# Kernel optimization log

Measured on AMD Instinct MI355X. Metric: run time of the kernel, lower is better.

The kernel has to match this reference:

```python
import jax, jax.numpy as jnp
import numpy as np
from jax import lax

HIDDEN = 30
NUM_CLASSES = 10
SEQ = 784
BATCH = 16384


def setup_inputs() -> dict:
    key = jax.random.key(0)
    k = jax.random.split(key, 6)
    s_ih = 1.0  # fan_in = 1
    s_hh = 1.0 / np.sqrt(HIDDEN)
    s_lin = 1.0 / np.sqrt(HIDDEN)
    return {
        "inputs": jax.random.normal(k[0], (BATCH, SEQ), dtype=jnp.float32),
        "W_ih": jax.random.normal(k[1], (HIDDEN, 1), dtype=jnp.float32) * s_ih,
        "W_hh": jax.random.normal(k[2], (HIDDEN, HIDDEN), dtype=jnp.float32) * s_hh,
        "b_mod": jax.random.normal(k[3], (HIDDEN,), dtype=jnp.float32) * 0.1,
        "W_lin": jax.random.normal(k[4], (NUM_CLASSES, HIDDEN), dtype=jnp.float32) * s_lin,
        "b_lin": jax.random.normal(k[5], (NUM_CLASSES,), dtype=jnp.float32) * s_lin,
    }


def reference(inputs, W_ih, W_hh, b_mod, W_lin, b_lin):
    # inputs: [B, 784] pixel-by-pixel sequence. Scan over the 784 time steps.
    B = inputs.shape[0]
    # Precompute the input projection for all steps at once: [784, B, H]
    # (W_ih has shape [H, 1], so x_t @ W_ih.T == x_t[:, None] * W_ih[:, 0])
    x_proj = inputs.T[:, :, None] * W_ih[:, 0][None, None, :]  # [784, B, H]

    def step(h, xp):
        z = xp + h @ W_hh.T  # [B, H]
        # modReLU: sign(z) * relu(|z| + b)
        h_new = jnp.sign(z) * jax.nn.relu(jnp.abs(z) + b_mod)
        return h_new, None

    h0 = jnp.zeros((B, HIDDEN), dtype=inputs.dtype)
    h_final, _ = lax.scan(step, h0, x_proj)
    return h_final @ W_lin.T + b_lin  # [B, 10] logits
```

## Files before the change

### kernel.cpp

```cpp
#include <hip/hip_runtime.h>
#include <stdint.h>

#define HID 30
#define NCLS 10
#define SEQ 784
#define NBATCH 16384
#define TCH 112
#define NSTAGE 7
#define XPAD 116

typedef _Float16 f16x8 __attribute__((ext_vector_type(8)));
typedef _Float16 f16x2 __attribute__((ext_vector_type(2)));
typedef float f32x4 __attribute__((ext_vector_type(4)));
typedef uint32_t u32x4 __attribute__((ext_vector_type(4)));

static __device__ __forceinline__ f16x8 mkfrag16(uint32_t a, uint32_t b, uint32_t c, uint32_t d) {
    u32x4 t = {a, b, c, d};
    return __builtin_bit_cast(f16x8, t);
}

static __device__ __forceinline__ uint32_t pkf16(_Float16 lo, _Float16 hi) {
    f16x2 v = {lo, hi};
    return __builtin_bit_cast(uint32_t, v);
}

static __device__ __forceinline__ uint32_t pk_rne(float a, float b) {
    return pkf16((_Float16)a, (_Float16)b);
}

static __device__ __forceinline__ uint32_t pkrtz(float a, float b) {
    return __builtin_bit_cast(uint32_t, __builtin_amdgcn_cvt_pkrtz(a, b));
}

static __device__ __forceinline__ uint32_t modrelu_pk(uint32_t z, uint32_t bp) {
    const f16x2 zero2 = {(_Float16)0.f, (_Float16)0.f};
    f16x2 t = __builtin_bit_cast(f16x2, z & 0x7FFF7FFFu) + __builtin_bit_cast(f16x2, bp);
    t = __builtin_elementwise_max(t, zero2);
    const uint32_t tb = __builtin_bit_cast(uint32_t, t);
    return (tb & 0x7FFF7FFFu) | (z & 0x80008000u);
}

static __device__ __forceinline__ uint32_t pkmax(uint32_t a, uint32_t b) {
    return __builtin_bit_cast(uint32_t,
        __builtin_elementwise_max(__builtin_bit_cast(f16x2, a), __builtin_bit_cast(f16x2, b)));
}

static __device__ __forceinline__ uint32_t scale_mul(uint32_t v, uint32_t sc32) {
    return __builtin_bit_cast(uint32_t,
        __builtin_bit_cast(f16x2, v) * __builtin_bit_cast(f16x2, sc32));
}

__launch_bounds__(64, 1)
__global__ void rnn_scan_kernel(const float* __restrict__ inp,
                                const float* __restrict__ W_ih,
                                const float* __restrict__ W_hh,
                                const float* __restrict__ b_mod,
                                const float* __restrict__ W_lin,
                                const float* __restrict__ b_lin,
                                float* __restrict__ out)
{
    __shared__ __align__(16) float xs_lds[16 * XPAD];

    const int lane = threadIdx.x;
    const int q = lane >> 4;
    const int n = lane & 15;
    const int b0 = blockIdx.x * 16;

    const int i1 = 8 * (n >> 2) + (n & 3);
    const int i2 = i1 + 4;

    uint32_t a1h[4], a1m[4], a2h[4], a2m[4];
    #pragma unroll
    for (int p = 0; p < 4; ++p) {
        _Float16 h1[2], m1[2], h2[2], m2[2];
        #pragma unroll
        for (int e = 0; e < 2; ++e) {
            const int j = 8 * q + 2 * p + e;
            float w1 = 0.f, w2 = 0.f;
            if (j < HID) {
                w1 = W_hh[i1 * HID + j];
                if (i2 < HID) w2 = W_hh[i2 * HID + j];
            } else if (j == HID) {
                w1 = W_ih[i1];
                if (i2 < HID) w2 = W_ih[i2];
            }
            h1[e] = (_Float16)w1; m1[e] = (_Float16)(w1 - (float)h1[e]);
            h2[e] = (_Float16)w2; m2[e] = (_Float16)(w2 - (float)h2[e]);
        }
        a1h[p] = pkf16(h1[0], h1[1]); a1m[p] = pkf16(m1[0], m1[1]);
        a2h[p] = pkf16(h2[0], h2[1]); a2m[p] = pkf16(m2[0], m2[1]);
    }
    const f16x8 A1h = mkfrag16(a1h[0], a1h[1], a1h[2], a1h[3]);
    const f16x8 A1m = mkfrag16(a1m[0], a1m[1], a1m[2], a1m[3]);
    const f16x8 A2h = mkfrag16(a2h[0], a2h[1], a2h[2], a2h[3]);
    const f16x8 A2m = mkfrag16(a2m[0], a2m[1], a2m[2], a2m[3]);

    uint32_t bSp[4];
    #pragma unroll
    for (int p = 0; p < 4; ++p) {
        const int ja = 8 * q + 2 * p;
        const int jb = ja + 1;
        const float ba = (ja < HID) ? b_mod[ja] : 0.f;
        const float bb = (jb < HID) ? b_mod[jb] : 0.f;
        bSp[p] = pk_rne(ba, bb);
    }

    uint32_t hp[4] = {0u, 0u, 0u, 0u};
    int xinv_e = 0;
    int pend_field = 15;

    const bool isq3 = (q == 3);
    const f32x4 z4 = {0.f, 0.f, 0.f, 0.f};

    auto do8 = [&](const uint32_t* xpk) {
        #pragma unroll
        for (int tt = 0; tt < 8; ++tt) {
            const f16x8 Bh = mkfrag16(hp[0], hp[1], hp[2], hp[3]);
            const f32x4 d1a = __builtin_amdgcn_mfma_f32_16x16x32_f16(A1h, Bh, z4, 0, 0, 0);
            const f32x4 d2a = __builtin_amdgcn_mfma_f32_16x16x32_f16(A2h, Bh, z4, 0, 0, 0);
            const f32x4 d1b = __builtin_amdgcn_mfma_f32_16x16x32_f16(A1m, Bh, z4, 0, 0, 0);
            const f32x4 d2b = __builtin_amdgcn_mfma_f32_16x16x32_f16(A2m, Bh, z4, 0, 0, 0);
            const f32x4 d1 = d1a + d1b;
            const f32x4 d2 = d2a + d2b;
            hp[0] = modrelu_pk(pk_rne(d1[0], d1[1]), bSp[0]);
            hp[1] = modrelu_pk(pk_rne(d1[2], d1[3]), bSp[1]);
            hp[2] = modrelu_pk(pk_rne(d2[0], d2[1]), bSp[2]);
            const uint32_t mr3 = modrelu_pk(pk_rne(d2[2], d2[3]), bSp[3]);
            hp[3] = isq3 ? xpk[(tt + 1) & 7] : mr3;
        }
    };

    for (int s = 0; s < NSTAGE; ++s) {
        #pragma unroll
        for (int r = 0; r < 7; ++r) {
            const int idx = r * 64 + lane;
            const int bl = idx / 28;
            const int t4 = idx % 28;
            const float4 v = *(const float4*)(inp + (size_t)(b0 + bl) * SEQ + s * TCH + t4 * 4);
            *(float4*)(&xs_lds[bl * XPAD + t4 * 4]) = v;
        }
        __syncthreads();

        const float* xrow = &xs_lds[n * XPAD];
        float4 xv0 = *(const float4*)(xrow);
        float4 xv1 = *(const float4*)(xrow + 4);

        for (int t16 = 0; t16 < 7; ++t16) {
            const uint32_t sc32 = (uint32_t)pend_field * 0x04000400u;
            #pragma unroll
            for (int p = 0; p < 4; ++p) hp[p] = scale_mul(hp[p], sc32);
            #pragma unroll
            for (int p = 0; p < 4; ++p) bSp[p] = scale_mul(bSp[p], sc32);
            xinv_e += pend_field - 15;

            const float fac = __uint_as_float((uint32_t)(127 + xinv_e) << 23);

            uint32_t mx;

            {
                const int toff = t16 * 16 + 8;
                const float4 xn0 = *(const float4*)(xrow + toff);
                const float4 xn1 = *(const float4*)(xrow + toff + 4);

                uint32_t xpk[8];
                xpk[0] = pkrtz(xv0.x * fac, 0.f); xpk[1] = pkrtz(xv0.y * fac, 0.f);
                xpk[2] = pkrtz(xv0.z * fac, 0.f); xpk[3] = pkrtz(xv0.w * fac, 0.f);
                xpk[4] = pkrtz(xv1.x * fac, 0.f); xpk[5] = pkrtz(xv1.y * fac, 0.f);
                xpk[6] = pkrtz(xv1.z * fac, 0.f); xpk[7] = pkrtz(xv1.w * fac, 0.f);
                hp[3] = isq3 ? xpk[0] : hp[3];

                mx = pkmax(pkmax(hp[0] & 0x7FFF7FFFu, hp[1] & 0x7FFF7FFFu),
                           pkmax(hp[2] & 0x7FFF7FFFu, hp[3] & 0x7FFF7FFFu));
                const uint32_t sh1 = (uint32_t)__shfl_xor((int)mx, 16);

                do8(xpk);

                mx = pkmax(mx, sh1);
                xv0 = xn0;
                xv1 = xn1;
            }
            const uint32_t sh2 = (uint32_t)__shfl_xor((int)mx, 32);

            {
                const int toff = (t16 < 6) ? (t16 + 1) * 16 : 0;
                const float4 xn0 = *(const float4*)(xrow + toff);
                const float4 xn1 = *(const float4*)(xrow + toff + 4);

                uint32_t xpk[8];
                xpk[0] = pkrtz(xv0.x * fac, 0.f); xpk[1] = pkrtz(xv0.y * fac, 0.f);
                xpk[2] = pkrtz(xv0.z * fac, 0.f); xpk[3] = pkrtz(xv0.w * fac, 0.f);
                xpk[4] = pkrtz(xv1.x * fac, 0.f); xpk[5] = pkrtz(xv1.y * fac, 0.f);
                xpk[6] = pkrtz(xv1.z * fac, 0.f); xpk[7] = pkrtz(xv1.w * fac, 0.f);
                hp[3] = isq3 ? xpk[0] : hp[3];

                do8(xpk);

                xv0 = xn0;
                xv1 = xn1;
            }

            mx = pkmax(mx, sh2);
            const uint32_t e16 = max(mx & 0xFFFFu, mx >> 16);
            const int e_raw = (int)(e16 >> 10);
            pend_field = min(max(25 - e_raw, 1), 20);
        }
        __syncthreads();
    }

    const float S = __uint_as_float((uint32_t)(127 - xinv_e) << 23);
    float hf[8];
    #pragma unroll
    for (int p = 0; p < 4; ++p) {
        const f16x2 v = __builtin_bit_cast(f16x2, hp[p]);
        hf[2 * p] = (float)v.x;
        hf[2 * p + 1] = (float)v.y;
    }
    float acc[NCLS];
    #pragma unroll
    for (int c = 0; c < NCLS; ++c) {
        float p = 0.f;
        #pragma unroll
        for (int k = 0; k < 8; ++k) {
            const int j = 8 * q + k;
            if (j < HID) p += W_lin[c * HID + j] * hf[k];
        }
        p += __shfl_xor(p, 16, 64);
        p += __shfl_xor(p, 32, 64);
        acc[c] = p * S + b_lin[c];
    }
    if (q == 0) {
        #pragma unroll
        for (int c = 0; c < NCLS; ++c)
            out[(size_t)(b0 + n) * NCLS + c] = acc[c];
    }
}

extern "C" void kernel_launch(void* const* d_in, const int* in_sizes, int n_in,
                              void* d_out, int out_size, void* d_ws, size_t ws_size,
                              hipStream_t stream) {
    const float* inp   = (const float*)d_in[0];
    const float* W_ih  = (const float*)d_in[1];
    const float* W_hh  = (const float*)d_in[2];
    const float* b_mod = (const float*)d_in[3];
    const float* W_lin = (const float*)d_in[4];
    const float* b_lin = (const float*)d_in[5];
    float* out = (float*)d_out;

    dim3 grid(NBATCH / 16);
    dim3 block(64);
    hipLaunchKernelGGL(rnn_scan_kernel, grid, block, 0, stream,
                       inp, W_ih, W_hh, b_mod, W_lin, b_lin, out);
}
```

Measured before the change: 191.2 us.

## Split recurrence rows across two waves with per-step LDS hidden-state exchange

Each block now runs two wavefronts. Each wave computes half of the hidden rows, so it issues two chained MFMAs per step instead of four. The new hidden-state halves are swapped through a double-buffered LDS array with a block barrier after every time step. The aim is to shorten the per-step MFMA critical path and double the number of resident waves. The cost is 784 block-wide barriers plus LDS write/read round trips on the serial dependency chain, and the end-of-stage barrier is removed.

```diff
diff --git a/kernel.cpp b/kernel.cpp
--- a/kernel.cpp
+++ b/kernel.cpp
@@ -50,7 +50,7 @@
         __builtin_bit_cast(f16x2, v) * __builtin_bit_cast(f16x2, sc32));
 }
 
-__launch_bounds__(64, 1)
+__launch_bounds__(128, 1)
 __global__ void rnn_scan_kernel(const float* __restrict__ inp,
                                 const float* __restrict__ W_ih,
                                 const float* __restrict__ W_hh,
@@ -60,84 +60,88 @@
                                 float* __restrict__ out)
 {
     __shared__ __align__(16) float xs_lds[16 * XPAD];
-
-    const int lane = threadIdx.x;
+    __shared__ uint32_t ex[2][4][64];
+
+    const int tid  = threadIdx.x;
+    const int wid  = tid >> 6;
+    const int lane = tid & 63;
     const int q = lane >> 4;
     const int n = lane & 15;
     const int b0 = blockIdx.x * 16;
 
-    const int i1 = 8 * (n >> 2) + (n & 3);
-    const int i2 = i1 + 4;
-
-    uint32_t a1h[4], a1m[4], a2h[4], a2m[4];
+    const int irow = 8 * (n >> 2) + (n & 3) + 4 * wid;
+
+    uint32_t ah[4], am[4];
     #pragma unroll
     for (int p = 0; p < 4; ++p) {
-        _Float16 h1[2], m1[2], h2[2], m2[2];
+        _Float16 hh[2], mm[2];
         #pragma unroll
         for (int e = 0; e < 2; ++e) {
             const int j = 8 * q + 2 * p + e;
-            float w1 = 0.f, w2 = 0.f;
-            if (j < HID) {
-                w1 = W_hh[i1 * HID + j];
-                if (i2 < HID) w2 = W_hh[i2 * HID + j];
-            } else if (j == HID) {
-                w1 = W_ih[i1];
-                if (i2 < HID) w2 = W_ih[i2];
-            }
-            h1[e] = (_Float16)w1; m1[e] = (_Float16)(w1 - (float)h1[e]);
-            h2[e] = (_Float16)w2; m2[e] = (_Float16)(w2 - (float)h2[e]);
-        }
-        a1h[p] = pkf16(h1[0], h1[1]); a1m[p] = pkf16(m1[0], m1[1]);
-        a2h[p] = pkf16(h2[0], h2[1]); a2m[p] = pkf16(m2[0], m2[1]);
-    }
-    const f16x8 A1h = mkfrag16(a1h[0], a1h[1], a1h[2], a1h[3]);
-    const f16x8 A1m = mkfrag16(a1m[0], a1m[1], a1m[2], a1m[3]);
-    const f16x8 A2h = mkfrag16(a2h[0], a2h[1], a2h[2], a2h[3]);
-    const f16x8 A2m = mkfrag16(a2m[0], a2m[1], a2m[2], a2m[3]);
-
-    uint32_t bSp[4];
-    #pragma unroll
-    for (int p = 0; p < 4; ++p) {
-        const int ja = 8 * q + 2 * p;
-        const int jb = ja + 1;
-        const float ba = (ja < HID) ? b_mod[ja] : 0.f;
-        const float bb = (jb < HID) ? b_mod[jb] : 0.f;
-        bSp[p] = pk_rne(ba, bb);
-    }
-
-    uint32_t hp[4] = {0u, 0u, 0u, 0u};
+            float w = 0.f;
+            if (irow < HID) {
+                if (j < HID) w = W_hh[irow * HID + j];
+                else if (j == HID) w = W_ih[irow];
+            }
+            hh[e] = (_Float16)w; mm[e] = (_Float16)(w - (float)hh[e]);
+        }
+        ah[p] = pkf16(hh[0], hh[1]); am[p] = pkf16(mm[0], mm[1]);
+    }
+    const f16x8 Ah = mkfrag16(ah[0], ah[1], ah[2], ah[3]);
+    const f16x8 Am = mkfrag16(am[0], am[1], am[2], am[3]);
+
+    uint32_t bS0, bS1;
+    {
+        const int r0 = 8 * q + 4 * wid;
+        const float ba = (r0     < HID) ? b_mod[r0]     : 0.f;
+        const float bb = (r0 + 1 < HID) ? b_mod[r0 + 1] : 0.f;
+        const float bc = (r0 + 2 < HID) ? b_mod[r0 + 2] : 0.f;
+        const float bd = (r0 + 3 < HID) ? b_mod[r0 + 3] : 0.f;
+        bS0 = pk_rne(ba, bb);
+        bS1 = pk_rne(bc, bd);
+    }
+
+    uint32_t B0 = 0u, B1 = 0u, B2 = 0u, B3 = 0u;
+    int par = 0;
     int xinv_e = 0;
     int pend_field = 15;
 
-    const bool isq3 = (q == 3);
+    const bool isq3  = (q == 3);
+    const bool isInj = (wid == 1) && isq3;
     const f32x4 z4 = {0.f, 0.f, 0.f, 0.f};
 
+    auto step = [&](uint32_t xnext) {
+        const f16x8 Bf = mkfrag16(B0, B1, B2, B3);
+        f32x4 d = __builtin_amdgcn_mfma_f32_16x16x32_f16(Ah, Bf, z4, 0, 0, 0);
+        d = __builtin_amdgcn_mfma_f32_16x16x32_f16(Am, Bf, d, 0, 0, 0);
+        const uint32_t u0  = modrelu_pk(pk_rne(d[0], d[1]), bS0);
+        const uint32_t u1m = modrelu_pk(pk_rne(d[2], d[3]), bS1);
+        const uint32_t u1  = isInj ? xnext : u1m;
+        ex[par][2 * wid][lane]     = u0;
+        ex[par][2 * wid + 1][lane] = u1;
+        __syncthreads();
+        B0 = ex[par][0][lane];
+        B1 = ex[par][1][lane];
+        B2 = ex[par][2][lane];
+        B3 = ex[par][3][lane];
+        par ^= 1;
+    };
+
     auto do8 = [&](const uint32_t* xpk) {
         #pragma unroll
-        for (int tt = 0; tt < 8; ++tt) {
-            const f16x8 Bh = mkfrag16(hp[0], hp[1], hp[2], hp[3]);
-            const f32x4 d1a = __builtin_amdgcn_mfma_f32_16x16x32_f16(A1h, Bh, z4, 0, 0, 0);
-            const f32x4 d2a = __builtin_amdgcn_mfma_f32_16x16x32_f16(A2h, Bh, z4, 0, 0, 0);
-            const f32x4 d1b = __builtin_amdgcn_mfma_f32_16x16x32_f16(A1m, Bh, z4, 0, 0, 0);
-            const f32x4 d2b = __builtin_amdgcn_mfma_f32_16x16x32_f16(A2m, Bh, z4, 0, 0, 0);
-            const f32x4 d1 = d1a + d1b;
-            const f32x4 d2 = d2a + d2b;
-            hp[0] = modrelu_pk(pk_rne(d1[0], d1[1]), bSp[0]);
-            hp[1] = modrelu_pk(pk_rne(d1[2], d1[3]), bSp[1]);
-            hp[2] = modrelu_pk(pk_rne(d2[0], d2[1]), bSp[2]);
-            const uint32_t mr3 = modrelu_pk(pk_rne(d2[2], d2[3]), bSp[3]);
-            hp[3] = isq3 ? xpk[(tt + 1) & 7] : mr3;
-        }
+        for (int tt = 0; tt < 8; ++tt) step(xpk[(tt + 1) & 7]);
     };
 
     for (int s = 0; s < NSTAGE; ++s) {
         #pragma unroll
-        for (int r = 0; r < 7; ++r) {
-            const int idx = r * 64 + lane;
-            const int bl = idx / 28;
-            const int t4 = idx % 28;
-            const float4 v = *(const float4*)(inp + (size_t)(b0 + bl) * SEQ + s * TCH + t4 * 4);
-            *(float4*)(&xs_lds[bl * XPAD + t4 * 4]) = v;
+        for (int r = 0; r < 4; ++r) {
+            const int idx = r * 128 + tid;
+            if (idx < 448) {
+                const int bl = idx / 28;
+                const int t4 = idx % 28;
+                const float4 v = *(const float4*)(inp + (size_t)(b0 + bl) * SEQ + s * TCH + t4 * 4);
+                *(float4*)(&xs_lds[bl * XPAD + t4 * 4]) = v;
+            }
         }
         __syncthreads();
 
@@ -147,10 +151,9 @@
 
         for (int t16 = 0; t16 < 7; ++t16) {
             const uint32_t sc32 = (uint32_t)pend_field * 0x04000400u;
-            #pragma unroll
-            for (int p = 0; p < 4; ++p) hp[p] = scale_mul(hp[p], sc32);
-            #pragma unroll
-            for (int p = 0; p < 4; ++p) bSp[p] = scale_mul(bSp[p], sc32);
+            B0 = scale_mul(B0, sc32); B1 = scale_mul(B1, sc32);
+            B2 = scale_mul(B2, sc32); B3 = scale_mul(B3, sc32);
+            bS0 = scale_mul(bS0, sc32); bS1 = scale_mul(bS1, sc32);
             xinv_e += pend_field - 15;
 
             const float fac = __uint_as_float((uint32_t)(127 + xinv_e) << 23);
@@ -167,10 +170,10 @@
                 xpk[2] = pkrtz(xv0.z * fac, 0.f); xpk[3] = pkrtz(xv0.w * fac, 0.f);
                 xpk[4] = pkrtz(xv1.x * fac, 0.f); xpk[5] = pkrtz(xv1.y * fac, 0.f);
                 xpk[6] = pkrtz(xv1.z * fac, 0.f); xpk[7] = pkrtz(xv1.w * fac, 0.f);
-                hp[3] = isq3 ? xpk[0] : hp[3];
-
-                mx = pkmax(pkmax(hp[0] & 0x7FFF7FFFu, hp[1] & 0x7FFF7FFFu),
-                           pkmax(hp[2] & 0x7FFF7FFFu, hp[3] & 0x7FFF7FFFu));
+                B3 = isq3 ? xpk[0] : B3;
+
+                mx = pkmax(pkmax(B0 & 0x7FFF7FFFu, B1 & 0x7FFF7FFFu),
+                           pkmax(B2 & 0x7FFF7FFFu, B3 & 0x7FFF7FFFu));
                 const uint32_t sh1 = (uint32_t)__shfl_xor((int)mx, 16);
 
                 do8(xpk);
@@ -191,7 +194,7 @@
                 xpk[2] = pkrtz(xv0.z * fac, 0.f); xpk[3] = pkrtz(xv0.w * fac, 0.f);
                 xpk[4] = pkrtz(xv1.x * fac, 0.f); xpk[5] = pkrtz(xv1.y * fac, 0.f);
                 xpk[6] = pkrtz(xv1.z * fac, 0.f); xpk[7] = pkrtz(xv1.w * fac, 0.f);
-                hp[3] = isq3 ? xpk[0] : hp[3];
+                B3 = isq3 ? xpk[0] : B3;
 
                 do8(xpk);
 
@@ -204,16 +207,19 @@
             const int e_raw = (int)(e16 >> 10);
             pend_field = min(max(25 - e_raw, 1), 20);
         }
-        __syncthreads();
     }
 
     const float S = __uint_as_float((uint32_t)(127 - xinv_e) << 23);
     float hf[8];
-    #pragma unroll
-    for (int p = 0; p < 4; ++p) {
-        const f16x2 v = __builtin_bit_cast(f16x2, hp[p]);
-        hf[2 * p] = (float)v.x;
-        hf[2 * p + 1] = (float)v.y;
+    {
+        const f16x2 v0 = __builtin_bit_cast(f16x2, B0);
+        const f16x2 v1 = __builtin_bit_cast(f16x2, B1);
+        const f16x2 v2 = __builtin_bit_cast(f16x2, B2);
+        const f16x2 v3 = __builtin_bit_cast(f16x2, B3);
+        hf[0] = (float)v0.x; hf[1] = (float)v0.y;
+        hf[2] = (float)v1.x; hf[3] = (float)v1.y;
+        hf[4] = (float)v2.x; hf[5] = (float)v2.y;
+        hf[6] = (float)v3.x; hf[7] = (float)v3.y;
     }
     float acc[NCLS];
     #pragma unroll
@@ -228,7 +234,7 @@
         p += __shfl_xor(p, 32, 64);
         acc[c] = p * S + b_lin[c];
     }
-    if (q == 0) {
+    if (wid == 0 && q == 0) {
         #pragma unroll
         for (int c = 0; c < NCLS; ++c)
             out[(size_t)(b0 + n) * NCLS + c] = acc[c];
@@ -247,7 +253,7 @@
     float* out = (float*)d_out;
 
     dim3 grid(NBATCH / 16);
-    dim3 block(64);
+    dim3 block(128);
     hipLaunchKernelGGL(rnn_scan_kernel, grid, block, 0, stream,
                        inp, W_ih, W_hh, b_mod, W_lin, b_lin, out);
 }
```

New measurement: 215.0 us. 12.5% more time.
